# Performance work log

Measured on AMD Instinct MI355X. Metric: run time of the kernel, lower is better.

## Reference

```python
import jax, jax.numpy as jnp
import numpy as np

# Config matching init_kwargs: input_shape=(C,T,H,W)=(512,32,14,14), window_size=9, n_heads=8
B, C, T, H, W = 2, 512, 32, 14, 14
N, K = 8, 9
CI = C // N              # per-head inter channels (64)
P = (K - 1) // 2         # symmetric temporal zero-pad so S == T


def setup_inputs() -> dict:
    key = jax.random.key(0)
    ks = jax.random.split(key, 7)
    s = 0.02
    return {
        "x":  jax.random.normal(ks[0], (B, C, T, H, W), jnp.float32),
        # per-head 1x1x1 conv (Linear3d) weights/biases, stacked over heads
        "Wq": jax.random.normal(ks[1], (N, CI, C), jnp.float32) * s,
        "bq": jax.random.normal(ks[2], (N, CI), jnp.float32) * s,
        "Wk": jax.random.normal(ks[3], (N, CI, C), jnp.float32) * s,
        "bk": jax.random.normal(ks[4], (N, CI), jnp.float32) * s,
        "Wv": jax.random.normal(ks[5], (N, CI, C), jnp.float32) * s,
        "bv": jax.random.normal(ks[6], (N, CI), jnp.float32) * s,
    }


def reference(x, Wq, bq, Wk, bk, Wv, bv):
    # x: (B, C, T, H, W). Dropout (p=0.25) is inference-mode identity.
    Bx, Cx, Tx, Hx, Wd = x.shape
    HW = Hx * Wd
    xf = x.reshape(Bx, Cx, Tx, HW)

    # Queries: every original frame is the center of its own window -> project x directly.
    q = jnp.einsum('bctp,nic->bnitp', xf, Wq) + bq[None, :, :, None, None]  # (B,N,ci,T,HW)

    # Keys/values on temporally zero-padded input (Pad3d gives S == T windows).
    xp = jnp.pad(xf, ((0, 0), (0, 0), (P, P), (0, 0)))  # (B,C,T+K-1,HW)
    k = jnp.einsum('bctp,nic->bnitp', xp, Wk) + bk[None, :, :, None, None]
    v = jnp.einsum('bctp,nic->bnitp', xp, Wv) + bv[None, :, :, None, None]

    # Sliding windows over padded time: window s covers padded frames s..s+K-1
    win = jnp.arange(Tx)[:, None] + jnp.arange(K)[None, :]  # (T,K)
    kw = k[:, :, :, win]  # (B,N,ci,T,K,HW)
    vw = v[:, :, :, win].reshape(Bx, N, CI, Tx, K * HW)

    # alpha[b,n,t,p,m] = sum_i q[b,n,i,t,p] * k_win[b,n,i,t,m]; softmax over keys m
    alpha = jnp.einsum('bnitp,bnitkm->bntpkm', q, kw).reshape(Bx, N, Tx, HW, K * HW)
    alpha = jax.nn.softmax(alpha, axis=-1)

    # y = alpha @ value -> (B,N,ci,T,HW); head concat is channel-major reshape
    y = jnp.einsum('bntpm,bnitm->bnitp', alpha, vw)
    z = y.reshape(Bx, Cx, Tx, Hx, Wd) + x  # residual
    return z
```

## Files before the change

### kernel.cpp

```cpp
#include <hip/hip_runtime.h>
#include <hip/hip_bf16.h>
#include <stdint.h>
#include <cstddef>

#define BB  2
#define CC  512
#define TT  32
#define HWP 196
#define NH  8
#define KWIN 9
#define CID 64
#define PPAD 4
#define TP  40
#define MTOT 12544
#define NTOT 1536
#define VSLOT 224
#define LOG2E 1.44269504f

typedef unsigned short u16;
typedef unsigned int   u32;
typedef __attribute__((ext_vector_type(8))) short short8;
typedef __attribute__((ext_vector_type(4))) float floatx4;

__device__ __forceinline__ u16 f2bf(float f) {
    u32 u = __float_as_uint(f);
    u32 r = (u + 0x7fffu + ((u >> 16) & 1u)) >> 16;
    return (u16)r;
}
__device__ __forceinline__ u32 pack2bf(float a, float b) {
    return (u32)f2bf(a) | ((u32)f2bf(b) << 16);
}
__device__ __forceinline__ u32 packtrunc(float a, float b) {
    return __builtin_amdgcn_perm(__float_as_uint(b), __float_as_uint(a), 0x07060302u);
}
__device__ __forceinline__ float fexp2(float x) {
    return __builtin_amdgcn_exp2f(x);
}
__device__ __forceinline__ void gload16(const u16* g, u16* l) {
    __builtin_amdgcn_global_load_lds(
        (const __attribute__((address_space(1))) u32*)g,
        (__attribute__((address_space(3))) u32*)l, 16, 0, 0);
}

__global__ __launch_bounds__(256) void prep_transpose(
    const float* __restrict__ x, u16* __restrict__ xt,
    const float* __restrict__ Wq, const float* __restrict__ Wk,
    const float* __restrict__ Wv, u16* __restrict__ Wbf,
    const float* __restrict__ bk, const float* __restrict__ bv,
    u16* __restrict__ Kout, u16* __restrict__ Vtp)
{
    __shared__ float T[64 * 197];
    int bxg = blockIdx.x;
    int tid = threadIdx.x;

    if (bxg < BB * TT * 8) {
        int bx = bxg;
        int ct = bx & 7; bx >>= 3;
        int t = bx & 31;
        int b = bx >> 5;
        const float* src = x + ((size_t)(b * CC + ct * 64) * TT + t) * HWP;
        for (int i = tid; i < 64 * 49; i += 256) {
            int c = i / 49;
            int p4 = i - c * 49;
            float4 v = *(const float4*)(src + (size_t)c * (TT * HWP) + p4 * 4);
            float* Tp = &T[c * 197 + p4 * 4];
            Tp[0] = v.x; Tp[1] = v.y; Tp[2] = v.z; Tp[3] = v.w;
        }
        __syncthreads();
        u16* dst = xt + (size_t)((b * TT + t) * HWP) * CC + ct * 64;
        for (int i = tid; i < HWP * 8; i += 256) {
            int p = i >> 3;
            int c0 = (i & 7) * 8;
            u32 w[4];
            #pragma unroll
            for (int k = 0; k < 4; k++)
                w[k] = pack2bf(T[(c0 + 2 * k) * 197 + p],
                               T[(c0 + 2 * k + 1) * 197 + p]);
            *(uint4*)(dst + (size_t)p * CC + c0) = *(uint4*)w;
        }
        return;
    }

    int id = (bxg - BB * TT * 8) * 256 + tid;
    const int wtot = NTOT * CC / 2;
    const int kper = 2 * NH * 8 * HWP * 32;
    const int vper = 2 * NH * 8 * 64 * (VSLOT/2);
    if (id < wtot) {
        int c2 = id & 255;
        int oc = id >> 8;
        int kind = oc >> 9;
        int idx = oc & 511;
        const float* src = (kind == 0 ? Wq : (kind == 1 ? Wk : Wv)) + (size_t)idx * CC + c2 * 2;
        ((u32*)Wbf)[id] = pack2bf(src[0], src[1]);
    } else if (id < wtot + kper) {
        int i = id - wtot;
        int ci2 = i & 31; i >>= 5;
        int p = i % HWP;  i /= HWP;
        int fr = i & 7;   i >>= 3;
        int head = i & 7;
        int b = i >> 3;
        int tp = fr < 4 ? fr : fr + 32;
        const float* bias = bk + head * CID + ci2 * 2;
        size_t addr = (((size_t)(b * NH + head) * TP + tp) * HWP + p) * 32 + ci2;
        ((u32*)Kout)[addr] = pack2bf(bias[0], bias[1]);
    } else if (id < wtot + kper + vper) {
        int i = id - wtot - kper;
        int s2 = i % (VSLOT/2); i /= (VSLOT/2);
        int ci = i & 63; i >>= 6;
        int fr = i & 7;  i >>= 3;
        int head = i & 7;
        int b = i >> 3;
        int tp = fr < 4 ? fr : fr + 32;
        float bias = bv[head * CID + ci];
        size_t addr = (((size_t)(b * NH + head) * TP + tp) * 64 + ci) * (VSLOT/2) + s2;
        ((u32*)Vtp)[addr] = pack2bf(bias, bias);
    }
}

__global__ __launch_bounds__(512) void proj_gemm2(
    const u16* __restrict__ xt, const u16* __restrict__ Wbf,
    const float* __restrict__ bq, const float* __restrict__ bk,
    const float* __restrict__ bv,
    u16* __restrict__ Qout, u16* __restrict__ Kout, u16* __restrict__ Vtp)
{
    __shared__ u16 sA[128 * 64];
    __shared__ u16 sB[256 * 64];

    int bx = blockIdx.x;
    int nb = bx % 6;
    int mt = bx / 6;
    int tid = threadIdx.x;
    int wave = tid >> 6, lane = tid & 63, quad = lane >> 4, l15 = lane & 15;
    int wm = wave >> 2, wn = wave & 3;
    int mbase = mt * 128 + wm * 64;
    int nbase = nb * 256 + wn * 64;

    int lr = lane >> 3;
    int sw = ((lane & 7) * 8) ^ (lr << 3);

    floatx4 acc[4][4];
    #pragma unroll
    for (int ms = 0; ms < 4; ms++)
        #pragma unroll
        for (int ns = 0; ns < 4; ns++)
            acc[ms][ns] = (floatx4){0.f, 0.f, 0.f, 0.f};

    const u16* abase = xt + (size_t)(mt * 128) * CC;
    const u16* bbase = Wbf + (size_t)(nb * 256) * CC;

    for (int kc = 0; kc < 8; kc++) {
        __syncthreads();
        #pragma unroll
        for (int i = 0; i < 2; i++) {
            int rbase = wave * 16 + i * 8;
            gload16(abase + (size_t)(rbase + lr) * CC + kc * 64 + sw,
                    &sA[rbase * 64]);
        }
        #pragma unroll
        for (int i = 0; i < 4; i++) {
            int rbase = wave * 32 + i * 8;
            gload16(bbase + (size_t)(rbase + lr) * CC + kc * 64 + sw,
                    &sB[rbase * 64]);
        }
        __syncthreads();

        #pragma unroll
        for (int kk = 0; kk < 2; kk++) {
            int swr = (kk * 32 + quad * 8) ^ ((l15 & 7) << 3);
            short8 af[4], bf[4];
            #pragma unroll
            for (int ms = 0; ms < 4; ms++)
                af[ms] = *(const short8*)&sA[(wm * 64 + ms * 16 + l15) * 64 + swr];
            #pragma unroll
            for (int ns = 0; ns < 4; ns++)
                bf[ns] = *(const short8*)&sB[(wn * 64 + ns * 16 + l15) * 64 + swr];
            #pragma unroll
            for (int ms = 0; ms < 4; ms++)
                #pragma unroll
                for (int ns = 0; ns < 4; ns++)
                    acc[ms][ns] = __builtin_amdgcn_mfma_f32_16x16x32_bf16(
                        af[ms], bf[ns], acc[ms][ns], 0, 0, 0);
        }
    }

    float biasv[4];
    #pragma unroll
    for (int ns = 0; ns < 4; ns++) {
        int n = nbase + ns * 16 + l15;
        int kind = n >> 9;
        int idx = n & 511;
        const float* bpb = kind == 0 ? bq : (kind == 1 ? bk : bv);
        biasv[ns] = bpb[idx];
    }

    #pragma unroll
    for (int ms = 0; ms < 4; ms++) {
        #pragma unroll
        for (int r = 0; r < 4; r++) {
            int m = mbase + ms * 16 + quad * 4 + r;
            int b = m / (TT * HWP);
            int rem = m - b * (TT * HWP);
            int t = rem / HWP;
            int p = rem - t * HWP;
            int slot_p = (p & ~31) | (p & 3) | (((p >> 4) & 1) << 2)
                       | (((p >> 2) & 1) << 3) | (((p >> 3) & 1) << 4);
            #pragma unroll
            for (int ns = 0; ns < 4; ns++) {
                int n = nbase + ns * 16 + l15;
                int kind = n >> 9;
                int idx = n & 511;
                int head = idx >> 6;
                int ci = idx & 63;
                float val = acc[ms][ns][r] + biasv[ns];
                if (kind == 0) {
                    Qout[(((size_t)(b * NH + head) * TT + t) * HWP + p) * CID + ci]
                        = f2bf(val * LOG2E);
                } else if (kind == 1) {
                    Kout[(((size_t)(b * NH + head) * TP + (t + PPAD)) * HWP + p) * CID + ci]
                        = f2bf(val);
                } else {
                    Vtp[(((size_t)(b * NH + head) * TP + (t + PPAD)) * 64 + ci) * VSLOT + slot_p]
                        = f2bf(val);
                }
            }
        }
    }
}

__global__ __launch_bounds__(256, 1) void attn_mfma4(
    const float* __restrict__ x,
    const u16* __restrict__ Qb, const u16* __restrict__ Kb,
    const u16* __restrict__ Vtp, float* __restrict__ zout)
{
    __shared__ union {
        struct { u16 K[26 * 512]; u16 V[28 * 512]; } s;
        struct { float eT[192 * 66]; float eT12[4][4][66]; float ls12[4][4]; } e;
    } u;

    int i = blockIdx.x;
    int xcd = i & 7;
    int r = i >> 3;
    int slab = ((r >= 32) ? 8 : 0) | xcd;
    int t = r & 31;
    int b = slab >> 3, n = slab & 7;

    int tid = threadIdx.x;
    int wave = tid >> 6;
    int lane = tid & 63;
    int quad = lane >> 4, l15 = lane & 15;
    int lr = lane >> 3;
    int ksw = ((lane & 7) * 8) ^ (lr << 3);

    const u16* kfr0 = Kb + (size_t)slab * (TP * HWP) * CID;
    const u16* vslab = Vtp + (size_t)slab * (TP * 64 * VSLOT);
    const float tmask = (quad == 0) ? 1.0f : 0.0f;

    short8 qf[3][2];
    #pragma unroll
    for (int j = 0; j < 3; j++) {
        int qrow = (wave + 4 * j) * 16 + l15;
        const u16* qp = Qb + ((size_t)(slab * TT + t) * HWP + qrow) * CID;
        qf[j][0] = *(const short8*)(qp + quad * 8);
        qf[j][1] = *(const short8*)(qp + 32 + quad * 8);
    }
    short8 qf12[2];
    {
        int qrow = 192 + l15;
        qrow = qrow < HWP ? qrow : (HWP - 1);
        const u16* qp = Qb + ((size_t)(slab * TT + t) * HWP + qrow) * CID;
        qf12[0] = *(const short8*)(qp + quad * 8);
        qf12[1] = *(const short8*)(qp + 32 + quad * 8);
    }

    floatx4 acc[3][4];
    floatx4 accl[3];
    floatx4 acc12[4];
    floatx4 accl12;
    #pragma unroll
    for (int j = 0; j < 3; j++) {
        #pragma unroll
        for (int cg = 0; cg < 4; cg++) acc[j][cg] = (floatx4){0.f, 0.f, 0.f, 0.f};
        accl[j] = (floatx4){0.f, 0.f, 0.f, 0.f};
    }
    #pragma unroll
    for (int cg = 0; cg < 4; cg++) acc12[cg] = (floatx4){0.f, 0.f, 0.f, 0.f};
    accl12 = (floatx4){0.f, 0.f, 0.f, 0.f};

    union { u32 w[4]; short8 s; } ones;
    ones.w[0] = 0x3F803F80u; ones.w[1] = 0x3F803F80u;
    ones.w[2] = 0x3F803F80u; ones.w[3] = 0x3F803F80u;

    #define KLOAD_L(c, D00, D01, D10, D11) do {                                  \
        int r0_ = (c) * 32 + l15;                                                \
        int sx_ = (l15 & 7) << 3;                                                \
        const u16* a0_ = &u.s.K[r0_ * 64];                                       \
        const u16* a1_ = &u.s.K[(r0_ + 16) * 64];                                \
        D00 = *(const short8*)(a0_ + ((quad * 8) ^ sx_));                        \
        D01 = *(const short8*)(a0_ + ((32 + quad * 8) ^ sx_));                   \
        D10 = *(const short8*)(a1_ + ((quad * 8) ^ sx_));                        \
        D11 = *(const short8*)(a1_ + ((32 + quad * 8) ^ sx_));                   \
    } while (0)

    #define KLOADTAIL_L(D00, D01) do {                                           \
        int r0_ = 192 + l15;                                                     \
        int sx_ = (l15 & 7) << 3;                                                \
        const u16* a0_ = &u.s.K[r0_ * 64];                                       \
        D00 = *(const short8*)(a0_ + ((quad * 8) ^ sx_));                        \
        D01 = *(const short8*)(a0_ + ((32 + quad * 8) ^ sx_));                   \
    } while (0)

    #define VLOAD_L(c, D0, D1, D2, D3) do {                                      \
        const u16* v_ = &u.s.V[l15 * VSLOT + (c) * 32 + quad * 8];               \
        D0 = *(const short8*)(v_);                                               \
        D1 = *(const short8*)(v_ + 16 * VSLOT);                                  \
        D2 = *(const short8*)(v_ + 32 * VSLOT);                                  \
        D3 = *(const short8*)(v_ + 48 * VSLOT);                                  \
    } while (0)

    #define CHUNK_ONE(Q0, Q1, ACC, ACCL, K00, K01, K10, K11, V0, V1, V2, V3) do {\
        floatx4 sc0 = (floatx4){0.f, 0.f, 0.f, 0.f};                             \
        sc0 = __builtin_amdgcn_mfma_f32_16x16x32_bf16(K00, Q0, sc0, 0, 0, 0);    \
        sc0 = __builtin_amdgcn_mfma_f32_16x16x32_bf16(K01, Q1, sc0, 0, 0, 0);    \
        floatx4 sc1 = (floatx4){0.f, 0.f, 0.f, 0.f};                             \
        sc1 = __builtin_amdgcn_mfma_f32_16x16x32_bf16(K10, Q0, sc1, 0, 0, 0);    \
        sc1 = __builtin_amdgcn_mfma_f32_16x16x32_bf16(K11, Q1, sc1, 0, 0, 0);    \
        union { u32 w[4]; short8 s; } pf;                                        \
        pf.w[0] = packtrunc(fexp2(sc0[0]), fexp2(sc0[1]));                       \
        pf.w[1] = packtrunc(fexp2(sc0[2]), fexp2(sc0[3]));                       \
        pf.w[2] = packtrunc(fexp2(sc1[0]), fexp2(sc1[1]));                       \
        pf.w[3] = packtrunc(fexp2(sc1[2]), fexp2(sc1[3]));                       \
        ACC[0] = __builtin_amdgcn_mfma_f32_16x16x32_bf16(pf.s, V0, ACC[0], 0, 0, 0); \
        ACC[1] = __builtin_amdgcn_mfma_f32_16x16x32_bf16(pf.s, V1, ACC[1], 0, 0, 0); \
        ACC[2] = __builtin_amdgcn_mfma_f32_16x16x32_bf16(pf.s, V2, ACC[2], 0, 0, 0); \
        ACC[3] = __builtin_amdgcn_mfma_f32_16x16x32_bf16(pf.s, V3, ACC[3], 0, 0, 0); \
        ACCL   = __builtin_amdgcn_mfma_f32_16x16x32_bf16(pf.s, ones.s, ACCL, 0, 0, 0); \
    } while (0)

    #define TAIL_ONE(Q0, Q1, ACC, ACCL, K00, K01, V0, V1, V2, V3) do {           \
        floatx4 sc0 = (floatx4){0.f, 0.f, 0.f, 0.f};                             \
        sc0 = __builtin_amdgcn_mfma_f32_16x16x32_bf16(K00, Q0, sc0, 0, 0, 0);    \
        sc0 = __builtin_amdgcn_mfma_f32_16x16x32_bf16(K01, Q1, sc0, 0, 0, 0);    \
        union { u32 w[4]; short8 s; } pf;                                        \
        pf.w[0] = packtrunc(fexp2(sc0[0]) * tmask, fexp2(sc0[1]) * tmask);       \
        pf.w[1] = packtrunc(fexp2(sc0[2]) * tmask, fexp2(sc0[3]) * tmask);       \
        pf.w[2] = 0u;                                                            \
        pf.w[3] = 0u;                                                            \
        ACC[0] = __builtin_amdgcn_mfma_f32_16x16x32_bf16(pf.s, V0, ACC[0], 0, 0, 0); \
        ACC[1] = __builtin_amdgcn_mfma_f32_16x16x32_bf16(pf.s, V1, ACC[1], 0, 0, 0); \
        ACC[2] = __builtin_amdgcn_mfma_f32_16x16x32_bf16(pf.s, V2, ACC[2], 0, 0, 0); \
        ACC[3] = __builtin_amdgcn_mfma_f32_16x16x32_bf16(pf.s, V3, ACC[3], 0, 0, 0); \
        ACCL   = __builtin_amdgcn_mfma_f32_16x16x32_bf16(pf.s, ones.s, ACCL, 0, 0, 0); \
    } while (0)

    #define CHUNK_FULL(K00, K01, K10, K11, V0, V1, V2, V3) do {                  \
        _Pragma("unroll")                                                        \
        for (int j = 0; j < 3; j++)                                              \
            CHUNK_ONE(qf[j][0], qf[j][1], acc[j], accl[j],                       \
                      K00, K01, K10, K11, V0, V1, V2, V3);                       \
        if (do12)                                                                \
            CHUNK_ONE(qf12[0], qf12[1], acc12, accl12,                           \
                      K00, K01, K10, K11, V0, V1, V2, V3);                       \
    } while (0)

    #define CHUNK_TAIL(K00, K01, V0, V1, V2, V3) do {                            \
        _Pragma("unroll")                                                        \
        for (int j = 0; j < 3; j++)                                              \
            TAIL_ONE(qf[j][0], qf[j][1], acc[j], accl[j],                        \
                     K00, K01, V0, V1, V2, V3);                                  \
        if (do12)                                                                \
            TAIL_ONE(qf12[0], qf12[1], acc12, accl12,                            \
                     K00, K01, V0, V1, V2, V3);                                  \
    } while (0)

    for (int f = 0; f < KWIN; f++) {
        int rbase = (t + f) * HWP;
        const u16* kfr = kfr0 + (size_t)rbase * CID;
        const u16* vfr = vslab + (size_t)(t + f) * (64 * VSLOT);
        bool do12 = ((f & 3) == wave);

        __syncthreads();
        #pragma unroll
        for (int it = 0; it < 14; it++) {
            int idx = it * 4 + wave;
            if (idx < 26) {
                gload16(kfr + (size_t)(idx * 8 + lr) * CID + ksw,
                        &u.s.K[idx * 512]);
            } else if (idx < 54) {
                int j2 = idx - 26;
                gload16(vfr + j2 * 512 + lane * 8, &u.s.V[j2 * 512]);
            }
        }
        __syncthreads();

        #pragma unroll
        for (int c = 0; c < 6; c++) {
            short8 k00, k01, k10, k11, v0, v1, v2, v3;
            KLOAD_L(c, k00, k01, k10, k11);
            VLOAD_L(c, v0, v1, v2, v3);
            CHUNK_FULL(k00, k01, k10, k11, v0, v1, v2, v3);
        }
        {
            short8 k00, k01, v0, v1, v2, v3;
            KLOADTAIL_L(k00, k01);
            VLOAD_L(6, v0, v1, v2, v3);
            CHUNK_TAIL(k00, k01, v0, v1, v2, v3);
        }
    }

    #undef KLOAD_L
    #undef KLOADTAIL_L
    #undef VLOAD_L
    #undef CHUNK_ONE
    #undef TAIL_ONE
    #undef CHUNK_FULL
    #undef CHUNK_TAIL

    __syncthreads();

    #pragma unroll
    for (int j = 0; j < 3; j++) {
        int tg = wave + 4 * j;
        float il[4];
        #pragma unroll
        for (int rr = 0; rr < 4; rr++) il[rr] = 1.0f / accl[j][rr];
        #pragma unroll
        for (int cg = 0; cg < 4; cg++) {
            #pragma unroll
            for (int rr = 0; rr < 4; rr++) {
                int p = tg * 16 + quad * 4 + rr;
                u.e.eT[p * 66 + cg * 16 + l15] = acc[j][cg][rr] * il[rr];
            }
        }
    }
    if (quad == 0) {
        #pragma unroll
        for (int rr = 0; rr < 4; rr++) {
            #pragma unroll
            for (int cg = 0; cg < 4; cg++)
                u.e.eT12[wave][rr][cg * 16 + l15] = acc12[cg][rr];
            if (l15 == 0) u.e.ls12[wave][rr] = accl12[rr];
        }
    }
    __syncthreads();

    if (tid < HWP) {
        size_t base = ((size_t)(b * CC + n * CID) * TT + t) * HWP + tid;
        if (tid < 192) {
            for (int ci = 0; ci < 64; ci++) {
                size_t a = base + (size_t)ci * (TT * HWP);
                zout[a] = u.e.eT[tid * 66 + ci] + x[a];
            }
        } else {
            int rr = tid - 192;
            float l = u.e.ls12[0][rr] + u.e.ls12[1][rr]
                    + u.e.ls12[2][rr] + u.e.ls12[3][rr];
            float il = 1.0f / l;
            for (int ci = 0; ci < 64; ci++) {
                size_t a = base + (size_t)ci * (TT * HWP);
                float v = (u.e.eT12[0][rr][ci] + u.e.eT12[1][rr][ci]
                         + u.e.eT12[2][rr][ci] + u.e.eT12[3][rr][ci]) * il;
                zout[a] = v + x[a];
            }
        }
    }
}

extern "C" void kernel_launch(void* const* d_in, const int* in_sizes, int n_in,
                              void* d_out, int out_size, void* d_ws, size_t ws_size,
                              hipStream_t stream) {
    const float* x  = (const float*)d_in[0];
    const float* Wq = (const float*)d_in[1];
    const float* bq = (const float*)d_in[2];
    const float* Wk = (const float*)d_in[3];
    const float* bk = (const float*)d_in[4];
    const float* Wv = (const float*)d_in[5];
    const float* bv = (const float*)d_in[6];
    float* z = (float*)d_out;

    const size_t qElems   = (size_t)BB * NH * TT * HWP * CID;
    const size_t kElems   = (size_t)BB * NH * TP * HWP * CID;
    const size_t vtpElems = (size_t)BB * NH * TP * 64 * VSLOT;

    u16* Qw  = (u16*)d_ws;
    u16* Kw  = Qw + qElems;
    u16* Vtp = Kw + kElems;
    u16* Wb  = Vtp + vtpElems;
    u16* Xt  = (u16*)d_out;

    {
        const int wtot = NTOT * CC / 2;
        const int kper = 2 * NH * 8 * HWP * 32;
        const int vper = 2 * NH * 8 * 64 * (VSLOT / 2);
        const int prepBlocks = (wtot + kper + vper + 255) / 256;
        prep_transpose<<<BB * TT * 8 + prepBlocks, 256, 0, stream>>>(
            x, Xt, Wq, Wk, Wv, Wb, bk, bv, Kw, Vtp);
    }
    proj_gemm2<<<98 * 6, 512, 0, stream>>>(Xt, Wb, bq, bk, bv, Qw, Kw, Vtp);
    attn_mfma4<<<512, 256, 0, stream>>>(x, Qw, Kw, Vtp, z);
}
```

Baseline: 213.0 us.

## Process two adjacent query frames per block to share staged K/V frames

Each attention block now handles two consecutive time steps with two 4-wave groups (512 threads), streaming 10 K/V frames through shared memory instead of 9 per time step. This is meant to cut global K/V traffic and the load-plus-barrier overhead per output frame by letting both groups reuse the same staged frame. In exchange, each group sits idle for one of the ten frame iterations, the grid halves to 256 blocks, which may underfill the CUs, and the epilogue is serialized over two phases with extra barriers.

```diff
diff --git a/kernel.cpp b/kernel.cpp
--- a/kernel.cpp
+++ b/kernel.cpp
@@ -227,7 +227,7 @@
     }
 }
 
-__global__ __launch_bounds__(256, 1) void attn_mfma4(
+__global__ __launch_bounds__(512, 1) void attn_mfma4(
     const float* __restrict__ x,
     const u16* __restrict__ Qb, const u16* __restrict__ Kb,
     const u16* __restrict__ Vtp, float* __restrict__ zout)
@@ -240,12 +240,16 @@
     int i = blockIdx.x;
     int xcd = i & 7;
     int r = i >> 3;
-    int slab = ((r >= 32) ? 8 : 0) | xcd;
-    int t = r & 31;
+    int slab = ((r >= 16) ? 8 : 0) | xcd;
+    int tpair = r & 15;
+    int t0 = tpair * 2;
     int b = slab >> 3, n = slab & 7;
 
     int tid = threadIdx.x;
     int wave = tid >> 6;
+    int grp = wave >> 2;
+    int wq = wave & 3;
+    int t = t0 + grp;
     int lane = tid & 63;
     int quad = lane >> 4, l15 = lane & 15;
     int lr = lane >> 3;
@@ -258,7 +262,7 @@
     short8 qf[3][2];
     #pragma unroll
     for (int j = 0; j < 3; j++) {
-        int qrow = (wave + 4 * j) * 16 + l15;
+        int qrow = (wq + 4 * j) * 16 + l15;
         const u16* qp = Qb + ((size_t)(slab * TT + t) * HWP + qrow) * CID;
         qf[j][0] = *(const short8*)(qp + quad * 8);
         qf[j][1] = *(const short8*)(qp + 32 + quad * 8);
@@ -372,16 +376,15 @@
                      K00, K01, V0, V1, V2, V3);                                  \
     } while (0)
 
-    for (int f = 0; f < KWIN; f++) {
-        int rbase = (t + f) * HWP;
-        const u16* kfr = kfr0 + (size_t)rbase * CID;
-        const u16* vfr = vslab + (size_t)(t + f) * (64 * VSLOT);
-        bool do12 = ((f & 3) == wave);
-
-        __syncthreads();
-        #pragma unroll
-        for (int it = 0; it < 14; it++) {
-            int idx = it * 4 + wave;
+    for (int fa = 0; fa < KWIN + 1; fa++) {
+        int af = t0 + fa;
+        const u16* kfr = kfr0 + (size_t)(af * HWP) * CID;
+        const u16* vfr = vslab + (size_t)af * (64 * VSLOT);
+
+        __syncthreads();
+        #pragma unroll
+        for (int it = 0; it < 7; it++) {
+            int idx = it * 8 + wave;
             if (idx < 26) {
                 gload16(kfr + (size_t)(idx * 8 + lr) * CID + ksw,
                         &u.s.K[idx * 512]);
@@ -392,18 +395,23 @@
         }
         __syncthreads();
 
-        #pragma unroll
-        for (int c = 0; c < 6; c++) {
-            short8 k00, k01, k10, k11, v0, v1, v2, v3;
-            KLOAD_L(c, k00, k01, k10, k11);
-            VLOAD_L(c, v0, v1, v2, v3);
-            CHUNK_FULL(k00, k01, k10, k11, v0, v1, v2, v3);
-        }
-        {
-            short8 k00, k01, v0, v1, v2, v3;
-            KLOADTAIL_L(k00, k01);
-            VLOAD_L(6, v0, v1, v2, v3);
-            CHUNK_TAIL(k00, k01, v0, v1, v2, v3);
+        bool active = (grp == 0) ? (fa < KWIN) : (fa >= 1);
+        int fr = fa - grp;
+        if (active) {
+            bool do12 = ((fr & 3) == wq);
+            #pragma unroll
+            for (int c = 0; c < 6; c++) {
+                short8 k00, k01, k10, k11, v0, v1, v2, v3;
+                KLOAD_L(c, k00, k01, k10, k11);
+                VLOAD_L(c, v0, v1, v2, v3);
+                CHUNK_FULL(k00, k01, k10, k11, v0, v1, v2, v3);
+            }
+            {
+                short8 k00, k01, v0, v1, v2, v3;
+                KLOADTAIL_L(k00, k01);
+                VLOAD_L(6, v0, v1, v2, v3);
+                CHUNK_TAIL(k00, k01, v0, v1, v2, v3);
+            }
         }
     }
 
@@ -418,50 +426,62 @@
     __syncthreads();
 
     #pragma unroll
-    for (int j = 0; j < 3; j++) {
-        int tg = wave + 4 * j;
-        float il[4];
-        #pragma unroll
-        for (int rr = 0; rr < 4; rr++) il[rr] = 1.0f / accl[j][rr];
-        #pragma unroll
-        for (int cg = 0; cg < 4; cg++) {
-            #pragma unroll
-            for (int rr = 0; rr < 4; rr++) {
-                int p = tg * 16 + quad * 4 + rr;
-                u.e.eT[p * 66 + cg * 16 + l15] = acc[j][cg][rr] * il[rr];
-            }
-        }
-    }
-    if (quad == 0) {
-        #pragma unroll
-        for (int rr = 0; rr < 4; rr++) {
-            #pragma unroll
-            for (int cg = 0; cg < 4; cg++)
-                u.e.eT12[wave][rr][cg * 16 + l15] = acc12[cg][rr];
-            if (l15 == 0) u.e.ls12[wave][rr] = accl12[rr];
-        }
-    }
-    __syncthreads();
-
-    if (tid < HWP) {
-        size_t base = ((size_t)(b * CC + n * CID) * TT + t) * HWP + tid;
-        if (tid < 192) {
-            for (int ci = 0; ci < 64; ci++) {
-                size_t a = base + (size_t)ci * (TT * HWP);
-                zout[a] = u.e.eT[tid * 66 + ci] + x[a];
-            }
-        } else {
-            int rr = tid - 192;
-            float l = u.e.ls12[0][rr] + u.e.ls12[1][rr]
-                    + u.e.ls12[2][rr] + u.e.ls12[3][rr];
-            float il = 1.0f / l;
-            for (int ci = 0; ci < 64; ci++) {
-                size_t a = base + (size_t)ci * (TT * HWP);
-                float v = (u.e.eT12[0][rr][ci] + u.e.eT12[1][rr][ci]
-                         + u.e.eT12[2][rr][ci] + u.e.eT12[3][rr][ci]) * il;
-                zout[a] = v + x[a];
-            }
-        }
+    for (int ph = 0; ph < 2; ph++) {
+        if (grp == ph) {
+            #pragma unroll
+            for (int j = 0; j < 3; j++) {
+                int tg = wq + 4 * j;
+                float il[4];
+                #pragma unroll
+                for (int rr = 0; rr < 4; rr++) il[rr] = 1.0f / accl[j][rr];
+                #pragma unroll
+                for (int cg = 0; cg < 4; cg++) {
+                    #pragma unroll
+                    for (int rr = 0; rr < 4; rr++) {
+                        int p = tg * 16 + quad * 4 + rr;
+                        u.e.eT[p * 66 + cg * 16 + l15] = acc[j][cg][rr] * il[rr];
+                    }
+                }
+            }
+            if (quad == 0) {
+                #pragma unroll
+                for (int rr = 0; rr < 4; rr++) {
+                    #pragma unroll
+                    for (int cg = 0; cg < 4; cg++)
+                        u.e.eT12[wq][rr][cg * 16 + l15] = acc12[cg][rr];
+                    if (l15 == 0) u.e.ls12[wq][rr] = accl12[rr];
+                }
+            }
+        }
+        __syncthreads();
+
+        {
+            int p = tid >> 1;
+            int ch = tid & 1;
+            if (p < HWP) {
+                size_t base = ((size_t)(b * CC + n * CID + ch * 32) * TT
+                               + (t0 + ph)) * HWP + p;
+                if (p < 192) {
+                    for (int ci = 0; ci < 32; ci++) {
+                        size_t a = base + (size_t)ci * (TT * HWP);
+                        zout[a] = u.e.eT[p * 66 + ch * 32 + ci] + x[a];
+                    }
+                } else {
+                    int rr = p - 192;
+                    float l = u.e.ls12[0][rr] + u.e.ls12[1][rr]
+                            + u.e.ls12[2][rr] + u.e.ls12[3][rr];
+                    float il = 1.0f / l;
+                    for (int ci = 0; ci < 32; ci++) {
+                        size_t a = base + (size_t)ci * (TT * HWP);
+                        int cc = ch * 32 + ci;
+                        float v = (u.e.eT12[0][rr][cc] + u.e.eT12[1][rr][cc]
+                                 + u.e.eT12[2][rr][cc] + u.e.eT12[3][rr][cc]) * il;
+                        zout[a] = v + x[a];
+                    }
+                }
+            }
+        }
+        __syncthreads();
     }
 }
 
@@ -496,5 +516,5 @@
             x, Xt, Wq, Wk, Wv, Wb, bk, bv, Kw, Vtp);
     }
     proj_gemm2<<<98 * 6, 512, 0, stream>>>(Xt, Wb, bq, bk, bv, Qw, Kw, Vtp);
-    attn_mfma4<<<512, 256, 0, stream>>>(x, Qw, Kw, Vtp, z);
-}
+    attn_mfma4<<<256, 512, 0, stream>>>(x, Qw, Kw, Vtp, z);
+}
```

New measurement: 215.4 us. About the same (+1.1%).
